# Kernel tuning notes

Hardware: AMD Instinct MI355X
Metric: run time of the kernel (lower is better)

## Reference

```python
import math
import jax, jax.numpy as jnp
import numpy as np

B, T = 2, 2048
D_MODEL, D_HEAD = 2048, 128
N_Q, N_KV = 16, 4
QPG = N_Q // N_KV  # queries per kv group
ROPE_BASE = 10000.0
YARN_SCALE = 4.0
ORIG_MAX_LEN = 4096
BETA_FAST, BETA_SLOW = 32.0, 1.0
RMS_EPS = 1.1920929e-07  # torch.finfo(float32).eps (nn.RMSNorm default)


def _yarn_inv_freq():
    inv = 1.0 / ROPE_BASE ** (np.arange(0, D_HEAD, 2, dtype=np.float32) / D_HEAD)
    wavelengths = 2.0 * math.pi / inv
    low_wavelen = ORIG_MAX_LEN / BETA_SLOW
    high_wavelen = ORIG_MAX_LEN / BETA_FAST
    gamma = np.clip((low_wavelen - wavelengths) / (low_wavelen - high_wavelen), 0.0, 1.0)
    return (gamma * inv + (1.0 - gamma) * inv / YARN_SCALE).astype(np.float32)

INV_FREQ = jnp.asarray(_yarn_inv_freq())  # (D_HEAD//2,) constant buffer
MSCALE = 0.1 * math.log(YARN_SCALE) + 1.0
ATTN_SCALE = 1.0 / (MSCALE * math.sqrt(D_HEAD))


def _rms_norm(x, w):
    # normalize over last dim (d_head), learnable per-dim weight
    return x * jax.lax.rsqrt(jnp.mean(x * x, axis=-1, keepdims=True) + RMS_EPS) * w


def _apply_rope(x):
    # x: (..., T, d_head)
    t = jnp.arange(x.shape[-2], dtype=jnp.float32)
    freqs = jnp.outer(t, INV_FREQ)                 # (T, d/2)
    emb = jnp.concatenate([freqs, freqs], axis=-1)  # (T, d)
    cos, sin = jnp.cos(emb), jnp.sin(emb)
    half = x.shape[-1] // 2
    x_rot = jnp.concatenate([-x[..., half:], x[..., :half]], axis=-1)
    return x * cos + x_rot * sin


def setup_inputs() -> dict:
    key = jax.random.key(0)
    ks = jax.random.split(key, 5)
    x = jax.random.normal(ks[0], (B, T, D_MODEL), dtype=jnp.float32)
    w_scale = 0.02
    Wq = jax.random.normal(ks[1], (D_MODEL, N_Q * D_HEAD), dtype=jnp.float32) * w_scale
    Wkv = jax.random.normal(ks[2], (D_MODEL, 2 * N_KV * D_HEAD), dtype=jnp.float32) * w_scale
    Wo = jax.random.normal(ks[3], (N_Q * D_HEAD, D_MODEL), dtype=jnp.float32) * w_scale
    q_norm_w = jnp.ones((D_HEAD,), dtype=jnp.float32)
    k_norm_w = jnp.ones((D_HEAD,), dtype=jnp.float32)
    return {"x": x, "Wq": Wq, "Wkv": Wkv, "Wo": Wo,
            "q_norm_w": q_norm_w, "k_norm_w": k_norm_w}


def reference(x, Wq, Wkv, Wo, q_norm_w, k_norm_w):
    b, t, _ = x.shape
    # projections
    q = (x @ Wq).reshape(b, t, QPG, N_KV, D_HEAD).transpose(0, 2, 3, 1, 4)  # (b,qpg,g,t,d)
    kv = x @ Wkv
    k, v = jnp.split(kv, 2, axis=-1)
    k = k.reshape(b, t, N_KV, D_HEAD).transpose(0, 2, 1, 3)  # (b,g,t,d)
    v = v.reshape(b, t, N_KV, D_HEAD).transpose(0, 2, 1, 3)  # (b,g,t,d)
    # RMSNorm + YaRN RoPE on q,k (math done in float32 as in source)
    q = _apply_rope(_rms_norm(q, q_norm_w))
    k = _apply_rope(_rms_norm(k, k_norm_w))
    # GQA replication: head index h = qpg*N_KV + g (matches source rearrange/reshape)
    q = q.reshape(b, N_Q, t, D_HEAD)
    k = jnp.broadcast_to(k[:, None], (b, QPG, N_KV, t, D_HEAD)).reshape(b, N_Q, t, D_HEAD)
    v = jnp.broadcast_to(v[:, None], (b, QPG, N_KV, t, D_HEAD)).reshape(b, N_Q, t, D_HEAD)
    # causal SDPA with custom scale
    scores = jnp.einsum('bhtd,bhsd->bhts', q, k) * ATTN_SCALE
    causal = jnp.tril(jnp.ones((t, t), dtype=bool))
    scores = jnp.where(causal, scores, jnp.finfo(scores.dtype).min)
    probs = jax.nn.softmax(scores, axis=-1)
    attn = jnp.einsum('bhts,bhsd->bhtd', probs, v)
    out = attn.transpose(0, 2, 1, 3).reshape(b, t, N_Q * D_HEAD)
    return out @ Wo
```

## Files before the change

### kernel.cpp

```cpp
#include <hip/hip_runtime.h>
#include <cmath>

typedef float f32x4 __attribute__((ext_vector_type(4)));
typedef __bf16 bf16x8 __attribute__((ext_vector_type(8)));

#define DEV static __device__ __forceinline__

DEV unsigned short f2bf(float f) {
  unsigned int u = __builtin_bit_cast(unsigned int, f);
  u += 0x7FFFu + ((u >> 16) & 1u);
  return (unsigned short)(u >> 16);
}
DEV float bf2f(unsigned short h) {
  unsigned int u = ((unsigned int)h) << 16;
  return __builtin_bit_cast(float, u);
}
DEV unsigned int cvtpk(float lo, float hi) {
  unsigned int r;
  asm("v_cvt_pk_bf16_f32 %0, %1, %2" : "=v"(r) : "v"(lo), "v"(hi));
  return r;
}
DEV f32x4 mfma16(bf16x8 a, bf16x8 b, f32x4 c) {
  return __builtin_amdgcn_mfma_f32_16x16x32_bf16(a, b, c, 0, 0, 0);
}
DEV void dma16(const void* g, void* l) {
  __builtin_amdgcn_global_load_lds(
      (const __attribute__((address_space(1))) void*)(uintptr_t)g,
      (__attribute__((address_space(3))) void*)(unsigned int)(uintptr_t)l,
      16, 0, 0);
}

constexpr int T_SEQ = 2048;

__global__ __launch_bounds__(256) void prep(const float4* __restrict__ in,
                                            ushort* __restrict__ out,
                                            float2* __restrict__ rope) {
  const int bx = blockIdx.x;
  if (bx < 8192) {
    int i = bx * 256 + threadIdx.x;
    float4 v = in[i];
    unsigned int lo = (unsigned int)f2bf(v.x) | ((unsigned int)f2bf(v.y) << 16);
    unsigned int hi = (unsigned int)f2bf(v.z) | ((unsigned int)f2bf(v.w) << 16);
    int row = i >> 9;
    int e = (i * 4) & 2047;
    size_t o = ((size_t)row << 11) + (size_t)(e ^ ((row & 7) << 3));
    *(uint2*)(out + o) = make_uint2(lo, hi);
  } else {
    int gid = (bx - 8192) * 256 + threadIdx.x;
    int t = gid >> 6, i = gid & 63;
    double inv = pow(10000.0, -((double)(2 * i)) / 128.0);
    double wl = 6.283185307179586 / inv;
    double gm = (4096.0 - wl) / (4096.0 - 128.0);
    gm = gm < 0.0 ? 0.0 : (gm > 1.0 ? 1.0 : gm);
    float f = (float)(gm * inv + (1.0 - gm) * inv * 0.25);
    float th = (float)t * f;
    float s, c;
    sincosf(th, &s, &c);
    rope[gid] = make_float2(c, s);
  }
}

__global__ __launch_bounds__(256) void tconv3(const float* __restrict__ Wq,
                                              const float* __restrict__ Wkv,
                                              const float* __restrict__ Wo,
                                              ushort* __restrict__ wqkv,
                                              ushort* __restrict__ wot) {
  __shared__ ushort tile[64][65];
  const int bx = blockIdx.x;
  const float* in;
  ushort* out;
  int C, bxl;
  if (bx < 32) {
    in = Wq; out = wqkv; C = 2048; bxl = bx;
  } else if (bx < 48) {
    in = Wkv; out = wqkv + (size_t)2048 * 2048; C = 1024; bxl = bx - 32;
  } else {
    in = Wo; out = wot; C = 2048; bxl = bx - 48;
  }
  const int R = 2048;
  int c0 = bxl * 64, r0 = blockIdx.y * 64;
  int j = threadIdx.x & 63, i0 = threadIdx.x >> 6;
#pragma unroll
  for (int ii = 0; ii < 16; ++ii) {
    int i = i0 + ii * 4;
    tile[i][j] = f2bf(in[(size_t)(r0 + i) * C + c0 + j]);
  }
  __syncthreads();
#pragma unroll
  for (int ii = 0; ii < 16; ++ii) {
    int jr = i0 + ii * 4;
    out[(size_t)(c0 + jr) * R + ((r0 + j) ^ ((jr & 7) << 3))] = tile[j][jr];
  }
}

template <int BM, int OUT_BF16>
__global__ __launch_bounds__(512) void gemm256(const ushort* __restrict__ A,
                                               const ushort* __restrict__ Bt,
                                               void* __restrict__ Cv,
                                               int M, int N, int K) {
  constexpr int MT = BM / 32;
  constexpr int NPH = MT / 2;
  constexpr int ADMA = BM / 64;
  __shared__ ushort lA[2][BM * 64];
  __shared__ ushort lB[2][256 * 64];
  const int tid = threadIdx.x, lane = tid & 63, w = tid >> 6;
  const int wm = (w >> 2) * (BM / 2);
  const int wn = (w & 3) * 64;
  const int m0 = blockIdx.y * BM, n0 = blockIdx.x * 256;

  f32x4 acc[MT][4] = {};

  const size_t K2 = (size_t)K * 2;
  const char* Ab = (const char*)A + (size_t)m0 * K2;
  const char* Bb = (const char*)Bt + (size_t)n0 * K2;
  const int srb = lane >> 3;
  const int scb = (lane & 7) * 16;

  auto stage = [&](int t, int bi) {
#pragma unroll
    for (int ii = 0; ii < ADMA; ++ii) {
      const int ar = w * (BM / 8) + ii * 8;
      dma16(Ab + (size_t)(ar + srb) * K2 + (size_t)t * 128 + scb,
            (char*)lA[bi] + ar * 128);
    }
#pragma unroll
    for (int ii = 0; ii < 4; ++ii) {
      const int br = w * 32 + ii * 8;
      dma16(Bb + (size_t)(br + srb) * K2 + (size_t)t * 128 + scb,
            (char*)lB[bi] + br * 128);
    }
  };

  stage(0, 0);
  const int nkt = K >> 6;

  for (int t = 0; t < nkt; ++t) {
    const int cur = t & 1;
    if (t + 1 < nkt) {
      stage(t + 1, cur ^ 1);
      if constexpr (BM == 256)
        asm volatile("s_waitcnt vmcnt(8)" ::: "memory");
      else
        asm volatile("s_waitcnt vmcnt(6)" ::: "memory");
    } else {
      asm volatile("s_waitcnt vmcnt(0)" ::: "memory");
    }
    __builtin_amdgcn_s_barrier();
    __builtin_amdgcn_sched_barrier(0);

    const char* lAc = (const char*)lA[cur];
    const char* lBc = (const char*)lB[cur];

#pragma unroll
    for (int ph = 0; ph < NPH; ++ph) {
      const int mb = (BM == 256) ? (ph >> 1) * 4 : 0;
      const int nb = (BM == 256) ? (ph & 1) * 2 : ph * 2;
#pragma unroll
      for (int kk = 0; kk < 2; ++kk) {
        bf16x8 af[4], bfr[2];
        const int byo = kk * 64 + ((lane >> 4) << 4);
#pragma unroll
        for (int i = 0; i < 4; ++i) {
          int row = wm + (mb + i) * 16 + (lane & 15);
          af[i] = *(const bf16x8*)(lAc + row * 128 + (byo ^ ((row & 7) << 4)));
        }
#pragma unroll
        for (int i = 0; i < 2; ++i) {
          int row = wn + (nb + i) * 16 + (lane & 15);
          bfr[i] = *(const bf16x8*)(lBc + row * 128 + (byo ^ ((row & 7) << 4)));
        }
        __builtin_amdgcn_s_setprio(1);
#pragma unroll
        for (int i = 0; i < 4; ++i)
#pragma unroll
          for (int j = 0; j < 2; ++j)
            acc[mb + i][nb + j] = mfma16(af[i], bfr[j], acc[mb + i][nb + j]);
        __builtin_amdgcn_s_setprio(0);
      }
    }
    __builtin_amdgcn_sched_barrier(0);
    __builtin_amdgcn_s_barrier();
  }

  const int rr = (lane >> 4) << 2;
  const int cc = lane & 15;
  if (OUT_BF16) {
    ushort* C = (ushort*)Cv;
#pragma unroll
    for (int mt = 0; mt < MT; ++mt)
#pragma unroll
      for (int nt = 0; nt < 4; ++nt)
#pragma unroll
        for (int j = 0; j < 4; ++j) {
          int r = m0 + wm + mt * 16 + rr + j;
          int c = n0 + wn + nt * 16 + cc;
          C[(size_t)r * N + c] = f2bf(acc[mt][nt][j]);
        }
  } else {
    float* C = (float*)Cv;
#pragma unroll
    for (int mt = 0; mt < MT; ++mt)
#pragma unroll
      for (int nt = 0; nt < 4; ++nt)
#pragma unroll
        for (int j = 0; j < 4; ++j) {
          int r = m0 + wm + mt * 16 + rr + j;
          int c = n0 + wn + nt * 16 + cc;
          C[(size_t)r * N + c] = acc[mt][nt][j];
        }
  }
}

__global__ __launch_bounds__(256) void norm_rope(const ushort* __restrict__ qkv,
                                                 const float* __restrict__ qw,
                                                 const float* __restrict__ kw,
                                                 const float2* __restrict__ rope,
                                                 ushort* __restrict__ qout,
                                                 ushort* __restrict__ kout,
                                                 float q_scale) {
  const int w = threadIdx.x >> 6, lane = threadIdx.x & 63;
  const int vi = blockIdx.x * 4 + w;
  const ushort* src;
  const float* wt;
  ushort* dst;
  float extra;
  int t, bb;
  if (vi < 65536) {
    int row = vi >> 4, H = vi & 15;
    bb = row >> 11;
    t = row & 2047;
    src = qkv + (size_t)row * 3072 + H * 128 + lane * 2;
    wt = qw;
    extra = q_scale;
    dst = qout + ((size_t)(bb * 16 + H) * T_SEQ + t) * 128 + lane * 2;
  } else {
    int vi2 = vi - 65536;
    int row = vi2 >> 2, gg = vi2 & 3;
    bb = row >> 11;
    t = row & 2047;
    src = qkv + (size_t)row * 3072 + 2048 + gg * 128 + lane * 2;
    wt = kw;
    extra = 1.f;
    dst = kout + ((size_t)(bb * 4 + gg) * T_SEQ + t) * 128 +
          ((lane * 2) ^ ((t & 7) << 3));
  }
  float x0 = bf2f(src[0]), x1 = bf2f(src[1]);
  float ss = x0 * x0 + x1 * x1;
#pragma unroll
  for (int d = 1; d < 64; d <<= 1) ss += __shfl_xor(ss, d, 64);
  float sc = rsqrtf(ss * (1.f / 128.f) + 1.1920929e-7f);
  float w0 = wt[lane * 2], w1 = wt[lane * 2 + 1];
  float xn0 = x0 * sc * w0, xn1 = x1 * sc * w1;
  float p0 = __shfl_xor(xn0, 32, 64), p1 = __shfl_xor(xn1, 32, 64);
  float r0 = lane < 32 ? -p0 : p0;
  float r1 = lane < 32 ? -p1 : p1;
  int i0 = (lane * 2) & 63;
  float2 cs0 = rope[t * 64 + i0];
  float2 cs1 = rope[t * 64 + i0 + 1];
  float o0 = (xn0 * cs0.x + r0 * cs0.y) * extra;
  float o1 = (xn1 * cs1.x + r1 * cs1.y) * extra;
  unsigned int pkv = (unsigned int)f2bf(o0) | ((unsigned int)f2bf(o1) << 16);
  *(unsigned int*)dst = pkv;
}

__global__ __launch_bounds__(256) void tv_kernel(const ushort* __restrict__ qkv,
                                                 ushort* __restrict__ vt) {
  __shared__ ushort tile[64][65];
  int t0 = blockIdx.x * 64;
  int y = blockIdx.y;
  int dh = y & 1, bg = y >> 1;
  int bb = bg >> 2, g = bg & 3;
  int j = threadIdx.x & 63, i0 = threadIdx.x >> 6;
#pragma unroll
  for (int ii = 0; ii < 16; ++ii) {
    int i = i0 + ii * 4;
    tile[i][j] = qkv[(size_t)(bb * T_SEQ + t0 + i) * 3072 + 2560 + g * 128 + dh * 64 + j];
  }
  __syncthreads();
#pragma unroll
  for (int ii = 0; ii < 16; ++ii) {
    int jr = i0 + ii * 4;
    vt[((size_t)bg * 128 + dh * 64 + jr) * T_SEQ + ((t0 + j) ^ ((jr & 7) << 3))] = tile[j][jr];
  }
}

__global__ __launch_bounds__(256, 2) void attn_fwd(const ushort* __restrict__ qh,
                                                   const ushort* __restrict__ kh,
                                                   const ushort* __restrict__ vt,
                                                   ushort* __restrict__ o) {
  const int f = blockIdx.x;
  const int half = f >> 8, c = f & 255;
  const int kk = c >> 5, bh = c & 31;
  const int qt = half ? kk : (15 - kk);
  const int b = bh >> 4, H = bh & 15;
  const int g = H & 3;
  const int tid = threadIdx.x, lane = tid & 63, w = tid >> 6;
  const int wrow0 = qt * 128 + w * 32;

  __shared__ ushort lK[2][64 * 128];
  __shared__ ushort lV[2][128 * 64];
  __shared__ ushort lP[4 * 32 * 64];

  bf16x8 qf[2][4];
#pragma unroll
  for (int mt = 0; mt < 2; ++mt) {
    const ushort* qb = qh + ((size_t)(b * 16 + H) * T_SEQ + wrow0 + mt * 16 + (lane & 15)) * 128 +
                       ((lane >> 4) << 3);
#pragma unroll
    for (int kc = 0; kc < 4; ++kc) qf[mt][kc] = *(const bf16x8*)(qb + kc * 32);
  }

  f32x4 oacc[2][8] = {};
  float mrow[2] = {-INFINITY, -INFINITY};
  float lrow[2] = {0.f, 0.f};

  const char* kpl = (const char*)(kh + (size_t)(b * 4 + g) * T_SEQ * 128);
  const char* vpl = (const char*)(vt + (size_t)(b * 4 + g) * 128 * T_SEQ);

  auto stage = [&](int j, int bi) {
#pragma unroll
    for (int ii = 0; ii < 4; ++ii) {
      const int off = w * 4096 + ii * 1024;
      dma16(kpl + (size_t)j * 16384 + off + lane * 16, (char*)lK[bi] + off);
      const int vrow = w * 32 + ii * 8 + (lane >> 3);
      dma16(vpl + (size_t)vrow * (T_SEQ * 2) + j * 128 + (lane & 7) * 16,
            (char*)lV[bi] + off);
    }
  };

  stage(0, 0);

  const int rsel = ((lane >> 4) << 2);

  const int jmax = 2 * qt + 1;
  for (int j = 0; j <= jmax; ++j) {
    const int cur = j & 1;
    if (j < jmax) {
      stage(j + 1, cur ^ 1);
      asm volatile("s_waitcnt vmcnt(8)" ::: "memory");
    } else {
      asm volatile("s_waitcnt vmcnt(0)" ::: "memory");
    }
    __builtin_amdgcn_s_barrier();
    __builtin_amdgcn_sched_barrier(0);

    f32x4 s[2][4];
#pragma unroll
    for (int nt = 0; nt < 4; ++nt) {
      bf16x8 kf[4];
      int krow = nt * 16 + (lane & 15);
#pragma unroll
      for (int kc = 0; kc < 4; ++kc) {
        int byo = kc * 64 + ((lane >> 4) << 4);
        kf[kc] = *(const bf16x8*)((const char*)lK[cur] + krow * 256 + (byo ^ ((krow & 7) << 4)));
      }
#pragma unroll
      for (int mt = 0; mt < 2; ++mt) {
        f32x4 a = {0.f, 0.f, 0.f, 0.f};
#pragma unroll
        for (int kc = 0; kc < 4; ++kc) a = mfma16(kf[kc], qf[mt][kc], a);
        s[mt][nt] = a;
      }
    }

    if (j * 64 + 63 > wrow0) {
#pragma unroll
      for (int mt = 0; mt < 2; ++mt) {
        int qrow = wrow0 + mt * 16 + (lane & 15);
#pragma unroll
        for (int nt = 0; nt < 4; ++nt)
#pragma unroll
          for (int jj = 0; jj < 4; ++jj) {
            int col = j * 64 + nt * 16 + rsel + jj;
            if (col > qrow) s[mt][nt][jj] = -3.0e38f;
          }
      }
    }

    float pmx[2], mn[2];
#pragma unroll
    for (int mt = 0; mt < 2; ++mt) {
      float a0 = fmaxf(fmaxf(s[mt][0][0], s[mt][0][1]), fmaxf(s[mt][0][2], s[mt][0][3]));
      float a1 = fmaxf(fmaxf(s[mt][1][0], s[mt][1][1]), fmaxf(s[mt][1][2], s[mt][1][3]));
      float a2 = fmaxf(fmaxf(s[mt][2][0], s[mt][2][1]), fmaxf(s[mt][2][2], s[mt][2][3]));
      float a3 = fmaxf(fmaxf(s[mt][3][0], s[mt][3][1]), fmaxf(s[mt][3][2], s[mt][3][3]));
      float p = fmaxf(fmaxf(a0, a1), fmaxf(a2, a3));
      p = fmaxf(p, __shfl_xor(p, 16, 64));
      p = fmaxf(p, __shfl_xor(p, 32, 64));
      pmx[mt] = p;
      mn[mt] = mrow[mt];
    }

    bool ok = (pmx[0] <= mrow[0] + 11.5417f) && (pmx[1] <= mrow[1] + 11.5417f);
    if (!__all(ok)) {
#pragma unroll
      for (int mt = 0; mt < 2; ++mt) {
        mn[mt] = fmaxf(mrow[mt], pmx[mt]);
        float rsc = exp2f(mrow[mt] - mn[mt]);
        mrow[mt] = mn[mt];
        lrow[mt] *= rsc;
        float rr0 = __shfl(rsc, rsel + 0, 64);
        float rr1 = __shfl(rsc, rsel + 1, 64);
        float rr2 = __shfl(rsc, rsel + 2, 64);
        float rr3 = __shfl(rsc, rsel + 3, 64);
#pragma unroll
        for (int dt = 0; dt < 8; ++dt) {
          oacc[mt][dt][0] *= rr0; oacc[mt][dt][1] *= rr1;
          oacc[mt][dt][2] *= rr2; oacc[mt][dt][3] *= rr3;
        }
      }
    }

#pragma unroll
    for (int mt = 0; mt < 2; ++mt) {
      float ps = 0.f;
      int prow = mt * 16 + (lane & 15);
      char* pbase = (char*)lP + w * 4096 + prow * 128;
      int swz = (prow & 7) << 4;
#pragma unroll
      for (int nt = 0; nt < 4; ++nt) {
        float p0 = exp2f(s[mt][nt][0] - mn[mt]);
        float p1 = exp2f(s[mt][nt][1] - mn[mt]);
        float p2 = exp2f(s[mt][nt][2] - mn[mt]);
        float p3 = exp2f(s[mt][nt][3] - mn[mt]);
        ps += (p0 + p1) + (p2 + p3);
        int pcb = (nt * 32 + ((lane >> 4) << 3)) ^ swz;
        *(uint2*)(pbase + pcb) = make_uint2(cvtpk(p0, p1), cvtpk(p2, p3));
      }
      ps += __shfl_xor(ps, 16, 64);
      ps += __shfl_xor(ps, 32, 64);
      lrow[mt] += ps;
    }

#pragma unroll
    for (int kc2 = 0; kc2 < 2; ++kc2) {
      bf16x8 pa[2];
#pragma unroll
      for (int mt = 0; mt < 2; ++mt) {
        int prow = mt * 16 + (lane & 15);
        int pbo = kc2 * 64 + ((lane >> 4) << 4);
        pa[mt] = *(const bf16x8*)((char*)lP + w * 4096 + prow * 128 + (pbo ^ ((prow & 7) << 4)));
      }
#pragma unroll
      for (int dt = 0; dt < 8; ++dt) {
        int vrow = dt * 16 + (lane & 15);
        int vbo = kc2 * 64 + ((lane >> 4) << 4);
        bf16x8 vf = *(const bf16x8*)((const char*)lV[cur] + vrow * 128 + (vbo ^ ((vrow & 7) << 4)));
#pragma unroll
        for (int mt = 0; mt < 2; ++mt) oacc[mt][dt] = mfma16(pa[mt], vf, oacc[mt][dt]);
      }
    }

    __builtin_amdgcn_sched_barrier(0);
    __builtin_amdgcn_s_barrier();
  }

#pragma unroll
  for (int mt = 0; mt < 2; ++mt) {
    float linv = 1.f / lrow[mt];
    float iv0 = __shfl(linv, rsel + 0, 64);
    float iv1 = __shfl(linv, rsel + 1, 64);
    float iv2 = __shfl(linv, rsel + 2, 64);
    float iv3 = __shfl(linv, rsel + 3, 64);
    int row = wrow0 + mt * 16 + rsel;
#pragma unroll
    for (int dt = 0; dt < 8; ++dt) {
      int col = H * 128 + dt * 16 + (lane & 15);
      o[(size_t)(b * T_SEQ + row + 0) * 2048 + (col ^ (((row + 0) & 7) << 3))] =
          f2bf(oacc[mt][dt][0] * iv0);
      o[(size_t)(b * T_SEQ + row + 1) * 2048 + (col ^ (((row + 1) & 7) << 3))] =
          f2bf(oacc[mt][dt][1] * iv1);
      o[(size_t)(b * T_SEQ + row + 2) * 2048 + (col ^ (((row + 2) & 7) << 3))] =
          f2bf(oacc[mt][dt][2] * iv2);
      o[(size_t)(b * T_SEQ + row + 3) * 2048 + (col ^ (((row + 3) & 7) << 3))] =
          f2bf(oacc[mt][dt][3] * iv3);
    }
  }
}

extern "C" void kernel_launch(void* const* d_in, const int* in_sizes, int n_in,
                              void* d_out, int out_size, void* d_ws, size_t ws_size,
                              hipStream_t stream) {
  (void)in_sizes; (void)n_in; (void)out_size; (void)ws_size;
  const float* x = (const float*)d_in[0];
  const float* Wq = (const float*)d_in[1];
  const float* Wkv = (const float*)d_in[2];
  const float* Wo = (const float*)d_in[3];
  const float* qnw = (const float*)d_in[4];
  const float* knw = (const float*)d_in[5];
  float* out = (float*)d_out;
  char* ws = (char*)d_ws;

  ushort* xb = (ushort*)(ws);
  ushort* wqkv = (ushort*)(ws + 16777216);
  ushort* wot = (ushort*)(ws + 29360128);
  ushort* qkvraw = (ushort*)(ws + 37748736);
  ushort* kh = (ushort*)(ws + 62914560);
  ushort* vtp = (ushort*)(ws + 67108864);
  float2* rope = (float2*)(ws + 71303168);
  ushort* qh = xb;
  ushort* attnb = qkvraw;

  float attn_scale = 1.0f / ((0.1f * logf(4.0f) + 1.0f) * sqrtf(128.0f));
  float q_scale = attn_scale * 1.44269504f;

  prep<<<8704, 256, 0, stream>>>((const float4*)x, xb, rope);
  tconv3<<<dim3(80, 32), 256, 0, stream>>>(Wq, Wkv, Wo, wqkv, wot);
  gemm256<256, 1><<<dim3(12, 16), 512, 0, stream>>>(xb, wqkv, qkvraw, 4096, 3072, 2048);
  norm_rope<<<20480, 256, 0, stream>>>(qkvraw, qnw, knw, rope, qh, kh, q_scale);
  tv_kernel<<<dim3(32, 16), 256, 0, stream>>>(qkvraw, vtp);
  attn_fwd<<<512, 256, 0, stream>>>(qh, kh, vtp, attnb);
  gemm256<128, 0><<<dim3(8, 32), 512, 0, stream>>>(attnb, wot, out, 4096, 2048, 2048);
}
```

Baseline: 214.9 us.

## Merge prep kernels, fuse norm-rope with V transpose, retile QKV GEMM

Merges the input/rope prep kernel with the weight transpose-convert kernel into one launch, and the norm+RoPE kernel with the V transpose into another, cutting launch count from 7 to 5. The QKV projection GEMM is generalized to a BN template parameter and switched from 256x256 tiles (192 blocks) to 128x384 tiles (256 blocks), which better fills the CUs. Risks include more registers per thread for the wider N accumulators and different LDS pressure.

```diff
diff --git a/kernel.cpp b/kernel.cpp
--- a/kernel.cpp
+++ b/kernel.cpp
@@ -32,9 +32,15 @@
 
 constexpr int T_SEQ = 2048;
 
-__global__ __launch_bounds__(256) void prep(const float4* __restrict__ in,
-                                            ushort* __restrict__ out,
-                                            float2* __restrict__ rope) {
+__global__ __launch_bounds__(256) void prep_all(const float4* __restrict__ in,
+                                                ushort* __restrict__ out,
+                                                float2* __restrict__ rope,
+                                                const float* __restrict__ Wq,
+                                                const float* __restrict__ Wkv,
+                                                const float* __restrict__ Wo,
+                                                ushort* __restrict__ wqkv,
+                                                ushort* __restrict__ wot) {
+  __shared__ ushort tile[64][65];
   const int bx = blockIdx.x;
   if (bx < 8192) {
     int i = bx * 256 + threadIdx.x;
@@ -45,7 +51,7 @@
     int e = (i * 4) & 2047;
     size_t o = ((size_t)row << 11) + (size_t)(e ^ ((row & 7) << 3));
     *(uint2*)(out + o) = make_uint2(lo, hi);
-  } else {
+  } else if (bx < 8704) {
     int gid = (bx - 8192) * 256 + threadIdx.x;
     int t = gid >> 6, i = gid & 63;
     double inv = pow(10000.0, -((double)(2 * i)) / 128.0);
@@ -57,58 +63,54 @@
     float s, c;
     sincosf(th, &s, &c);
     rope[gid] = make_float2(c, s);
-  }
-}
-
-__global__ __launch_bounds__(256) void tconv3(const float* __restrict__ Wq,
-                                              const float* __restrict__ Wkv,
-                                              const float* __restrict__ Wo,
-                                              ushort* __restrict__ wqkv,
-                                              ushort* __restrict__ wot) {
-  __shared__ ushort tile[64][65];
-  const int bx = blockIdx.x;
-  const float* in;
-  ushort* out;
-  int C, bxl;
-  if (bx < 32) {
-    in = Wq; out = wqkv; C = 2048; bxl = bx;
-  } else if (bx < 48) {
-    in = Wkv; out = wqkv + (size_t)2048 * 2048; C = 1024; bxl = bx - 32;
   } else {
-    in = Wo; out = wot; C = 2048; bxl = bx - 48;
-  }
-  const int R = 2048;
-  int c0 = bxl * 64, r0 = blockIdx.y * 64;
-  int j = threadIdx.x & 63, i0 = threadIdx.x >> 6;
-#pragma unroll
-  for (int ii = 0; ii < 16; ++ii) {
-    int i = i0 + ii * 4;
-    tile[i][j] = f2bf(in[(size_t)(r0 + i) * C + c0 + j]);
-  }
-  __syncthreads();
-#pragma unroll
-  for (int ii = 0; ii < 16; ++ii) {
-    int jr = i0 + ii * 4;
-    out[(size_t)(c0 + jr) * R + ((r0 + j) ^ ((jr & 7) << 3))] = tile[j][jr];
-  }
-}
-
-template <int BM, int OUT_BF16>
+    const int l = bx - 8704;
+    const int bxl0 = l % 80, by = l / 80;
+    const float* src;
+    ushort* dst;
+    int C, bxl;
+    if (bxl0 < 32) {
+      src = Wq; dst = wqkv; C = 2048; bxl = bxl0;
+    } else if (bxl0 < 48) {
+      src = Wkv; dst = wqkv + (size_t)2048 * 2048; C = 1024; bxl = bxl0 - 32;
+    } else {
+      src = Wo; dst = wot; C = 2048; bxl = bxl0 - 48;
+    }
+    const int R = 2048;
+    int c0 = bxl * 64, r0 = by * 64;
+    int j = threadIdx.x & 63, i0 = threadIdx.x >> 6;
+#pragma unroll
+    for (int ii = 0; ii < 16; ++ii) {
+      int i = i0 + ii * 4;
+      tile[i][j] = f2bf(src[(size_t)(r0 + i) * C + c0 + j]);
+    }
+    __syncthreads();
+#pragma unroll
+    for (int ii = 0; ii < 16; ++ii) {
+      int jr = i0 + ii * 4;
+      dst[(size_t)(c0 + jr) * R + ((r0 + j) ^ ((jr & 7) << 3))] = tile[j][jr];
+    }
+  }
+}
+
+template <int BM, int BN, int OUT_BF16>
 __global__ __launch_bounds__(512) void gemm256(const ushort* __restrict__ A,
                                                const ushort* __restrict__ Bt,
                                                void* __restrict__ Cv,
                                                int M, int N, int K) {
   constexpr int MT = BM / 32;
-  constexpr int NPH = MT / 2;
+  constexpr int NT = BN / 64;
+  constexpr int NPH = (MT / 4) * (NT / 2);
   constexpr int ADMA = BM / 64;
+  constexpr int BDMA = BN / 64;
   __shared__ ushort lA[2][BM * 64];
-  __shared__ ushort lB[2][256 * 64];
+  __shared__ ushort lB[2][BN * 64];
   const int tid = threadIdx.x, lane = tid & 63, w = tid >> 6;
   const int wm = (w >> 2) * (BM / 2);
-  const int wn = (w & 3) * 64;
-  const int m0 = blockIdx.y * BM, n0 = blockIdx.x * 256;
-
-  f32x4 acc[MT][4] = {};
+  const int wn = (w & 3) * (BN / 4);
+  const int m0 = blockIdx.y * BM, n0 = blockIdx.x * BN;
+
+  f32x4 acc[MT][NT] = {};
 
   const size_t K2 = (size_t)K * 2;
   const char* Ab = (const char*)A + (size_t)m0 * K2;
@@ -124,8 +126,8 @@
             (char*)lA[bi] + ar * 128);
     }
 #pragma unroll
-    for (int ii = 0; ii < 4; ++ii) {
-      const int br = w * 32 + ii * 8;
+    for (int ii = 0; ii < BDMA; ++ii) {
+      const int br = w * (BN / 8) + ii * 8;
       dma16(Bb + (size_t)(br + srb) * K2 + (size_t)t * 128 + scb,
             (char*)lB[bi] + br * 128);
     }
@@ -138,10 +140,12 @@
     const int cur = t & 1;
     if (t + 1 < nkt) {
       stage(t + 1, cur ^ 1);
-      if constexpr (BM == 256)
+      if constexpr (ADMA + BDMA == 8)
         asm volatile("s_waitcnt vmcnt(8)" ::: "memory");
+      else if constexpr (ADMA + BDMA == 6)
+        asm volatile("s_waitcnt vmcnt(6)" ::: "memory");
       else
-        asm volatile("s_waitcnt vmcnt(6)" ::: "memory");
+        asm volatile("s_waitcnt vmcnt(4)" ::: "memory");
     } else {
       asm volatile("s_waitcnt vmcnt(0)" ::: "memory");
     }
@@ -153,8 +157,8 @@
 
 #pragma unroll
     for (int ph = 0; ph < NPH; ++ph) {
-      const int mb = (BM == 256) ? (ph >> 1) * 4 : 0;
-      const int nb = (BM == 256) ? (ph & 1) * 2 : ph * 2;
+      const int mb = (ph / (NT / 2)) * 4;
+      const int nb = (ph % (NT / 2)) * 2;
 #pragma unroll
       for (int kk = 0; kk < 2; ++kk) {
         bf16x8 af[4], bfr[2];
@@ -189,7 +193,7 @@
 #pragma unroll
     for (int mt = 0; mt < MT; ++mt)
 #pragma unroll
-      for (int nt = 0; nt < 4; ++nt)
+      for (int nt = 0; nt < NT; ++nt)
 #pragma unroll
         for (int j = 0; j < 4; ++j) {
           int r = m0 + wm + mt * 16 + rr + j;
@@ -201,7 +205,7 @@
 #pragma unroll
     for (int mt = 0; mt < MT; ++mt)
 #pragma unroll
-      for (int nt = 0; nt < 4; ++nt)
+      for (int nt = 0; nt < NT; ++nt)
 #pragma unroll
         for (int j = 0; j < 4; ++j) {
           int r = m0 + wm + mt * 16 + rr + j;
@@ -211,76 +215,78 @@
   }
 }
 
-__global__ __launch_bounds__(256) void norm_rope(const ushort* __restrict__ qkv,
-                                                 const float* __restrict__ qw,
-                                                 const float* __restrict__ kw,
-                                                 const float2* __restrict__ rope,
-                                                 ushort* __restrict__ qout,
-                                                 ushort* __restrict__ kout,
-                                                 float q_scale) {
-  const int w = threadIdx.x >> 6, lane = threadIdx.x & 63;
-  const int vi = blockIdx.x * 4 + w;
-  const ushort* src;
-  const float* wt;
-  ushort* dst;
-  float extra;
-  int t, bb;
-  if (vi < 65536) {
-    int row = vi >> 4, H = vi & 15;
-    bb = row >> 11;
-    t = row & 2047;
-    src = qkv + (size_t)row * 3072 + H * 128 + lane * 2;
-    wt = qw;
-    extra = q_scale;
-    dst = qout + ((size_t)(bb * 16 + H) * T_SEQ + t) * 128 + lane * 2;
+__global__ __launch_bounds__(256) void normrope_tv(const ushort* __restrict__ qkv,
+                                                   const float* __restrict__ qw,
+                                                   const float* __restrict__ kw,
+                                                   const float2* __restrict__ rope,
+                                                   ushort* __restrict__ qout,
+                                                   ushort* __restrict__ kout,
+                                                   ushort* __restrict__ vt,
+                                                   float q_scale) {
+  __shared__ ushort tile[64][65];
+  const int bx = blockIdx.x;
+  if (bx < 20480) {
+    const int w = threadIdx.x >> 6, lane = threadIdx.x & 63;
+    const int vi = bx * 4 + w;
+    const ushort* src;
+    const float* wt;
+    ushort* dst;
+    float extra;
+    int t, bb;
+    if (vi < 65536) {
+      int row = vi >> 4, H = vi & 15;
+      bb = row >> 11;
+      t = row & 2047;
+      src = qkv + (size_t)row * 3072 + H * 128 + lane * 2;
+      wt = qw;
+      extra = q_scale;
+      dst = qout + ((size_t)(bb * 16 + H) * T_SEQ + t) * 128 + lane * 2;
+    } else {
+      int vi2 = vi - 65536;
+      int row = vi2 >> 2, gg = vi2 & 3;
+      bb = row >> 11;
+      t = row & 2047;
+      src = qkv + (size_t)row * 3072 + 2048 + gg * 128 + lane * 2;
+      wt = kw;
+      extra = 1.f;
+      dst = kout + ((size_t)(bb * 4 + gg) * T_SEQ + t) * 128 +
+            ((lane * 2) ^ ((t & 7) << 3));
+    }
+    float x0 = bf2f(src[0]), x1 = bf2f(src[1]);
+    float ss = x0 * x0 + x1 * x1;
+#pragma unroll
+    for (int d = 1; d < 64; d <<= 1) ss += __shfl_xor(ss, d, 64);
+    float sc = rsqrtf(ss * (1.f / 128.f) + 1.1920929e-7f);
+    float w0 = wt[lane * 2], w1 = wt[lane * 2 + 1];
+    float xn0 = x0 * sc * w0, xn1 = x1 * sc * w1;
+    float p0 = __shfl_xor(xn0, 32, 64), p1 = __shfl_xor(xn1, 32, 64);
+    float r0 = lane < 32 ? -p0 : p0;
+    float r1 = lane < 32 ? -p1 : p1;
+    int i0 = (lane * 2) & 63;
+    float2 cs0 = rope[t * 64 + i0];
+    float2 cs1 = rope[t * 64 + i0 + 1];
+    float o0 = (xn0 * cs0.x + r0 * cs0.y) * extra;
+    float o1 = (xn1 * cs1.x + r1 * cs1.y) * extra;
+    unsigned int pkv = (unsigned int)f2bf(o0) | ((unsigned int)f2bf(o1) << 16);
+    *(unsigned int*)dst = pkv;
   } else {
-    int vi2 = vi - 65536;
-    int row = vi2 >> 2, gg = vi2 & 3;
-    bb = row >> 11;
-    t = row & 2047;
-    src = qkv + (size_t)row * 3072 + 2048 + gg * 128 + lane * 2;
-    wt = kw;
-    extra = 1.f;
-    dst = kout + ((size_t)(bb * 4 + gg) * T_SEQ + t) * 128 +
-          ((lane * 2) ^ ((t & 7) << 3));
-  }
-  float x0 = bf2f(src[0]), x1 = bf2f(src[1]);
-  float ss = x0 * x0 + x1 * x1;
-#pragma unroll
-  for (int d = 1; d < 64; d <<= 1) ss += __shfl_xor(ss, d, 64);
-  float sc = rsqrtf(ss * (1.f / 128.f) + 1.1920929e-7f);
-  float w0 = wt[lane * 2], w1 = wt[lane * 2 + 1];
-  float xn0 = x0 * sc * w0, xn1 = x1 * sc * w1;
-  float p0 = __shfl_xor(xn0, 32, 64), p1 = __shfl_xor(xn1, 32, 64);
-  float r0 = lane < 32 ? -p0 : p0;
-  float r1 = lane < 32 ? -p1 : p1;
-  int i0 = (lane * 2) & 63;
-  float2 cs0 = rope[t * 64 + i0];
-  float2 cs1 = rope[t * 64 + i0 + 1];
-  float o0 = (xn0 * cs0.x + r0 * cs0.y) * extra;
-  float o1 = (xn1 * cs1.x + r1 * cs1.y) * extra;
-  unsigned int pkv = (unsigned int)f2bf(o0) | ((unsigned int)f2bf(o1) << 16);
-  *(unsigned int*)dst = pkv;
-}
-
-__global__ __launch_bounds__(256) void tv_kernel(const ushort* __restrict__ qkv,
-                                                 ushort* __restrict__ vt) {
-  __shared__ ushort tile[64][65];
-  int t0 = blockIdx.x * 64;
-  int y = blockIdx.y;
-  int dh = y & 1, bg = y >> 1;
-  int bb = bg >> 2, g = bg & 3;
-  int j = threadIdx.x & 63, i0 = threadIdx.x >> 6;
-#pragma unroll
-  for (int ii = 0; ii < 16; ++ii) {
-    int i = i0 + ii * 4;
-    tile[i][j] = qkv[(size_t)(bb * T_SEQ + t0 + i) * 3072 + 2560 + g * 128 + dh * 64 + j];
-  }
-  __syncthreads();
-#pragma unroll
-  for (int ii = 0; ii < 16; ++ii) {
-    int jr = i0 + ii * 4;
-    vt[((size_t)bg * 128 + dh * 64 + jr) * T_SEQ + ((t0 + j) ^ ((jr & 7) << 3))] = tile[j][jr];
+    const int l = bx - 20480;
+    int t0 = (l & 31) * 64;
+    int y = l >> 5;
+    int dh = y & 1, bg = y >> 1;
+    int bb = bg >> 2, g = bg & 3;
+    int j = threadIdx.x & 63, i0 = threadIdx.x >> 6;
+#pragma unroll
+    for (int ii = 0; ii < 16; ++ii) {
+      int i = i0 + ii * 4;
+      tile[i][j] = qkv[(size_t)(bb * T_SEQ + t0 + i) * 3072 + 2560 + g * 128 + dh * 64 + j];
+    }
+    __syncthreads();
+#pragma unroll
+    for (int ii = 0; ii < 16; ++ii) {
+      int jr = i0 + ii * 4;
+      vt[((size_t)bg * 128 + dh * 64 + jr) * T_SEQ + ((t0 + j) ^ ((jr & 7) << 3))] = tile[j][jr];
+    }
   }
 }
 
@@ -504,11 +510,9 @@
   float attn_scale = 1.0f / ((0.1f * logf(4.0f) + 1.0f) * sqrtf(128.0f));
   float q_scale = attn_scale * 1.44269504f;
 
-  prep<<<8704, 256, 0, stream>>>((const float4*)x, xb, rope);
-  tconv3<<<dim3(80, 32), 256, 0, stream>>>(Wq, Wkv, Wo, wqkv, wot);
-  gemm256<256, 1><<<dim3(12, 16), 512, 0, stream>>>(xb, wqkv, qkvraw, 4096, 3072, 2048);
-  norm_rope<<<20480, 256, 0, stream>>>(qkvraw, qnw, knw, rope, qh, kh, q_scale);
-  tv_kernel<<<dim3(32, 16), 256, 0, stream>>>(qkvraw, vtp);
+  prep_all<<<11264, 256, 0, stream>>>((const float4*)x, xb, rope, Wq, Wkv, Wo, wqkv, wot);
+  gemm256<128, 384, 1><<<dim3(8, 32), 512, 0, stream>>>(xb, wqkv, qkvraw, 4096, 3072, 2048);
+  normrope_tv<<<20992, 256, 0, stream>>>(qkvraw, qnw, knw, rope, qh, kh, vtp, q_scale);
   attn_fwd<<<512, 256, 0, stream>>>(qh, kh, vtp, attnb);
-  gemm256<128, 0><<<dim3(8, 32), 512, 0, stream>>>(attnb, wot, out, 4096, 2048, 2048);
-}
+  gemm256<128, 256, 0><<<dim3(8, 32), 512, 0, stream>>>(attnb, wot, out, 4096, 2048, 2048);
+}
```

New measurement: 201.1 us. 1.07x faster.
